# Kernel optimization log

Measured on AMD Instinct MI355X. Metric: run time of the kernel, lower is better.

## Reference

```python
import jax, jax.numpy as jnp
import numpy as np

B, N, E = 32, 2000, 32000      # graphs, nodes/graph, edges/graph
V, D, R, K = 100000, 128, 39, 8  # vocab, emb_dim, n_relation, n_bases
EPS = 1e-5


def setup_inputs() -> dict:
    key = jax.random.key(0)
    ks = jax.random.split(key, 8)
    node_ids = jax.random.randint(ks[0], (B, N), 0, V)
    edge_index = jax.random.randint(ks[1], (B, 2, E), 0, N)
    edge_type = jax.random.randint(ks[2], (B, E), 0, R)
    embedding = jax.random.normal(ks[3], (V, D), jnp.float32) * D ** -0.5
    bases = jax.random.normal(ks[4], (K, D, D), jnp.float32) * D ** -0.5
    comp = jax.random.normal(ks[5], (R, K), jnp.float32) * K ** -0.5
    root = jax.random.normal(ks[6], (D, D), jnp.float32) * D ** -0.5
    bias = jnp.zeros((D,), jnp.float32)
    return dict(node_ids=node_ids, edge_index=edge_index, edge_type=edge_type,
                embedding=embedding, bases=bases, comp=comp, root=root, bias=bias)


def _graph_fwd(node_ids, edge_index, edge_type, embedding, bases, comp, root, bias):
    # RGCNConv with basis decomposition and per-relation MEAN aggregation (PyG default).
    x = embedding[node_ids]                       # [N, D] per-graph node features
    src, dst = edge_index[0], edge_index[1]       # j -> i, aggregate at dst
    x_src = x[src]                                # [E, D]
    # mean normalizer per (dst, relation) bucket
    comb = dst * R + edge_type                    # [E]
    cnt = jax.ops.segment_sum(jnp.ones((E,), jnp.float32), comb, num_segments=N * R)
    inv = jnp.where(cnt > 0, 1.0 / cnt, 0.0)[comb]  # [E]
    # W_r = sum_k comp[r,k] * bases[k]; fold comp coefficients + mean norm into edge weights
    w = comp[edge_type] * inv[:, None]            # [E, K]
    out = x @ root + bias                         # root/self connection
    for k in range(K):                            # small fixed loop over bases
        zk = jax.ops.segment_sum(w[:, k:k + 1] * x_src, dst, num_segments=N)  # [N, D]
        out = out + zk @ bases[k]
    g = out.sum(axis=0)                           # sum pool over nodes
    # torch.nn.functional.normalize(p=2, eps=1e-5)
    return g / jnp.maximum(jnp.linalg.norm(g), EPS)


def reference(node_ids, edge_index, edge_type, embedding, bases, comp, root, bias):
    f = jax.vmap(_graph_fwd, in_axes=(0, 0, 0, None, None, None, None, None))
    return f(node_ids, edge_index, edge_type, embedding, bases, comp, root, bias)  # [B, D]
```

## Files before the change

### kernel.cpp

```cpp
#include <hip/hip_runtime.h>
#include <math.h>

#define Bn 32
#define Nn 2000
#define En 32000
#define Vn 100000
#define Dn 128
#define Rn 39
#define Kn 8

#define SUBS 8
#define NPS (Nn / SUBS)
#define NPAIR (Nn / 2)
#define EQ (En / 4)
#define NR (NPS * Rn)
#define GBLK 16
#define WSLOT (GBLK * 8)


__global__ __launch_bounds__(1024) void cntinv_kernel(const int* __restrict__ edge_index,
                                                      const int* __restrict__ edge_type,
                                                      float* __restrict__ inv) {
    int b = blockIdx.x, sub = blockIdx.y;
    int base = sub * NR;
    __shared__ int loc[NR];
    for (int i = threadIdx.x; i < NR; i += 1024) loc[i] = 0;
    __syncthreads();
    const int4* dst4 = (const int4*)(edge_index + (b * 2 + 1) * En);
    const int4* et4  = (const int4*)(edge_type + b * En);
    for (int q = threadIdx.x; q < EQ; q += 1024) {
        int4 d = dst4[q]; int4 t = et4[q]; int y;
        y = d.x * Rn + t.x - base; if ((unsigned)y < NR) atomicAdd(&loc[y], 1);
        y = d.y * Rn + t.y - base; if ((unsigned)y < NR) atomicAdd(&loc[y], 1);
        y = d.z * Rn + t.z - base; if ((unsigned)y < NR) atomicAdd(&loc[y], 1);
        y = d.w * Rn + t.w - base; if ((unsigned)y < NR) atomicAdd(&loc[y], 1);
    }
    __syncthreads();
    float* finv = (float*)loc;
    for (int i = threadIdx.x; i < NR; i += 1024) {
        int c = loc[i];
        finv[i] = 1.0f / (float)c;
    }
    __syncthreads();
    float* ivb = inv + (size_t)b * En;
    for (int q = threadIdx.x; q < EQ; q += 1024) {
        int4 d = dst4[q]; int4 t = et4[q];
        int e = 4 * q, y;
        y = d.x * Rn + t.x - base; if ((unsigned)y < NR) ivb[e]     = finv[y];
        y = d.y * Rn + t.y - base; if ((unsigned)y < NR) ivb[e + 1] = finv[y];
        y = d.z * Rn + t.z - base; if ((unsigned)y < NR) ivb[e + 2] = finv[y];
        y = d.w * Rn + t.w - base; if ((unsigned)y < NR) ivb[e + 3] = finv[y];
    }
}

__global__ __launch_bounds__(1024) void a_kernel(const int* __restrict__ edge_index,
                                                 const int* __restrict__ edge_type,
                                                 const float* __restrict__ inv,
                                                 const float* __restrict__ comp,
                                                 float* __restrict__ a) {
    int b = blockIdx.x, sub = blockIdx.y;
    int base = sub * NR;
    __shared__ float s[NR];
    __shared__ float comp_l[Rn * Kn];
    for (int i = threadIdx.x; i < NR; i += 1024) s[i] = 0.0f;
    if (threadIdx.x < Rn * Kn) comp_l[threadIdx.x] = comp[threadIdx.x];
    __syncthreads();
    const int4*   src4 = (const int4*)(edge_index + (b * 2 + 0) * En);
    const int4*   et4  = (const int4*)(edge_type + b * En);
    const float4* iv4  = (const float4*)(inv + (size_t)b * En);
    for (int q = threadIdx.x; q < EQ; q += 1024) {
        int4 sv = src4[q]; int4 tv = et4[q]; float4 iv = iv4[q]; int y;
        y = sv.x * Rn + tv.x - base; if ((unsigned)y < NR) atomicAdd(&s[y], iv.x);
        y = sv.y * Rn + tv.y - base; if ((unsigned)y < NR) atomicAdd(&s[y], iv.y);
        y = sv.z * Rn + tv.z - base; if ((unsigned)y < NR) atomicAdd(&s[y], iv.z);
        y = sv.w * Rn + tv.w - base; if ((unsigned)y < NR) atomicAdd(&s[y], iv.w);
    }
    __syncthreads();
    float* g = a + ((size_t)b * Nn + sub * NPS) * Kn;
    for (int i = threadIdx.x; i < NPS * Kn; i += 1024) {
        int n = i >> 3, k = i & 7;
        float acc = 0.0f;
        const float* srow = &s[n * Rn];
        for (int t = 0; t < Rn; t++) acc += srow[t] * comp_l[t * Kn + k];
        g[i] = acc;
    }
}

__global__ __launch_bounds__(512, 4) void gather_kernel(const int* __restrict__ node_ids,
                                                        const float* __restrict__ emb,
                                                        const float* __restrict__ a,
                                                        float* __restrict__ partial) {
    int b = blockIdx.x;
    int lane = threadIdx.x & 63, wv = threadIdx.x >> 6;
    int Wl = blockIdx.y * 8 + wv;
    int half = lane >> 5;
    int dl = lane & 31;
    __shared__ float red[8][9][Dn];
    float4 acc[9];
#pragma unroll
    for (int k = 0; k < 9; k++) acc[k] = make_float4(0.f, 0.f, 0.f, 0.f);
    const int*   nb = node_ids + b * Nn;
    const float* ab = a + (size_t)b * Nn * Kn;
#pragma unroll
    for (int i0 = 0; i0 < 8; i0 += 4) {
        bool   has[4];
        int    node[4];
        float4 v[4];
        float4 a0[4], a1[4];
#pragma unroll
        for (int i = 0; i < 4; i++) {
            int p = Wl + (i0 + i) * WSLOT;
            has[i] = p < NPAIR;
            node[i] = (has[i] ? 2 * p : 0) + half;
        }
#pragma unroll
        for (int i = 0; i < 4; i++) {
            int nid = nb[node[i]];
            v[i] = has[i] ? ((const float4*)(emb + (size_t)nid * Dn))[dl]
                          : make_float4(0.f, 0.f, 0.f, 0.f);
            const float4* ar = (const float4*)(ab + (size_t)node[i] * Kn);
            a0[i] = ar[0]; a1[i] = ar[1];
        }
#pragma unroll
        for (int i = 0; i < 4; i++) {
            float w[9] = {a0[i].x, a0[i].y, a0[i].z, a0[i].w,
                          a1[i].x, a1[i].y, a1[i].z, a1[i].w, 1.0f};
#pragma unroll
            for (int k = 0; k < 9; k++) {
                acc[k].x += w[k] * v[i].x;
                acc[k].y += w[k] * v[i].y;
                acc[k].z += w[k] * v[i].z;
                acc[k].w += w[k] * v[i].w;
            }
        }
    }
#pragma unroll
    for (int k = 0; k < 9; k++) {
        acc[k].x += __shfl_down(acc[k].x, 32, 64);
        acc[k].y += __shfl_down(acc[k].y, 32, 64);
        acc[k].z += __shfl_down(acc[k].z, 32, 64);
        acc[k].w += __shfl_down(acc[k].w, 32, 64);
    }
    if (half == 0) {
#pragma unroll
        for (int k = 0; k < 9; k++)
            ((float4*)red[wv][k])[dl] = acc[k];
    }
    __syncthreads();
    int slot = threadIdx.x;
    if (slot < 9 * (Dn / 4)) {
        int k = slot >> 5, d4 = slot & 31;
        float4 t = make_float4(0.f, 0.f, 0.f, 0.f);
#pragma unroll
        for (int w = 0; w < 8; w++) {
            float4 v = ((const float4*)red[w][k])[d4];
            t.x += v.x; t.y += v.y; t.z += v.z; t.w += v.w;
        }
        float4* gp = (float4*)(partial + (((size_t)b * 9 + k) * GBLK + blockIdx.y) * Dn);
        gp[d4] = t;
    }
}

__global__ __launch_bounds__(256) void matvec_kernel(const float* __restrict__ partial,
                                                     const float* __restrict__ root,
                                                     const float* __restrict__ bases,
                                                     float* __restrict__ gmat) {
    int b = blockIdx.x, m = blockIdx.y;
    int tid = threadIdx.x;
    __shared__ float4 ts4[Dn / 4];
    __shared__ float tsh[8][Dn];
    int dg = tid & 31, part = tid >> 5;
    const float4* p4 = (const float4*)(partial + ((size_t)b * 9 + m) * GBLK * Dn);
    float4 sum = make_float4(0.f, 0.f, 0.f, 0.f);
    for (int c = part; c < GBLK; c += 8) {
        float4 v = p4[c * 32 + dg];
        sum.x += v.x; sum.y += v.y; sum.z += v.z; sum.w += v.w;
    }
    ((float4*)tsh[part])[dg] = sum;
    __syncthreads();
    if (part == 0) {
        float4 t = make_float4(0.f, 0.f, 0.f, 0.f);
#pragma unroll
        for (int r = 0; r < 8; r++) {
            float4 v = ((float4*)tsh[r])[dg];
            t.x += v.x; t.y += v.y; t.z += v.z; t.w += v.w;
        }
        ts4[dg] = t;
    }
    __syncthreads();
    const float* ts = (const float*)ts4;
    const float* M  = (m == 8) ? root : bases + (size_t)m * Dn * Dn;
    int d = tid & (Dn - 1), h = tid >> 7;
    float g = 0.0f;
#pragma unroll 8
    for (int j = h * 64; j < h * 64 + 64; j++) g += ts[j] * M[j * Dn + d];
    __syncthreads();
    tsh[h][d] = g;
    __syncthreads();
    if (h == 0) gmat[((size_t)b * 9 + m) * Dn + d] = tsh[0][d] + tsh[1][d];
}

__global__ __launch_bounds__(128) void norm_kernel(const float* __restrict__ gmat,
                                                   const float* __restrict__ bias,
                                                   float* __restrict__ out) {
    int b = blockIdx.x, d = threadIdx.x;
    float g = (float)Nn * bias[d];
    const float* gb = gmat + (size_t)b * 9 * Dn + d;
#pragma unroll
    for (int m = 0; m < 9; m++) g += gb[m * Dn];
    float ss = g * g;
#pragma unroll
    for (int off = 32; off > 0; off >>= 1) ss += __shfl_down(ss, off, 64);
    __shared__ float s2[2];
    if ((threadIdx.x & 63) == 0) s2[threadIdx.x >> 6] = ss;
    __syncthreads();
    float nrm = sqrtf(s2[0] + s2[1]);
    out[b * Dn + d] = g / fmaxf(nrm, 1e-5f);
}

extern "C" void kernel_launch(void* const* d_in, const int* in_sizes, int n_in,
                              void* d_out, int out_size, void* d_ws, size_t ws_size,
                              hipStream_t stream) {
    const int*   node_ids   = (const int*)d_in[0];
    const int*   edge_index = (const int*)d_in[1];
    const int*   edge_type  = (const int*)d_in[2];
    const float* embedding  = (const float*)d_in[3];
    const float* bases      = (const float*)d_in[4];
    const float* comp       = (const float*)d_in[5];
    const float* root       = (const float*)d_in[6];
    const float* bias       = (const float*)d_in[7];
    float*       out        = (float*)d_out;

    char* w = (char*)d_ws;
    float* inv     = (float*)(w + 0);
    float* a       = (float*)(w + 4096000);
    float* partial = (float*)(w + 6144000);
    float* gmat    = (float*)(w + 8503296);

    cntinv_kernel<<<dim3(Bn, SUBS), 1024, 0, stream>>>(edge_index, edge_type, inv);
    a_kernel     <<<dim3(Bn, SUBS), 1024, 0, stream>>>(edge_index, edge_type, inv, comp, a);
    gather_kernel<<<dim3(Bn, GBLK), 512,  0, stream>>>(node_ids, embedding, a, partial);
    matvec_kernel<<<dim3(Bn, 9),    256,  0, stream>>>(partial, root, bases, gmat);
    norm_kernel  <<<Bn, 128, 0, stream>>>(gmat, bias, out);
}
```

Measured before the change: 141.4 us.

## Fuse all stages into one cooperative persistent kernel with grid syncs

Replaces the five separate launches (count/inverse, per-node coefficients, embedding gather, matvec, normalize) with one cooperative kernel of 256 blocks of 1024 threads. Stages are separated by grid.sync, and the gather now uses 16 waves per block over 8 sub-blocks per graph. The final matvec and normalize are merged into a single per-graph stage that runs on the first 32 blocks. This removes the launch gaps and intermediate gmat traffic, but adds grid-wide barrier costs and fixes the block shape for every stage.

```diff
diff --git a/kernel.cpp b/kernel.cpp
--- a/kernel.cpp
+++ b/kernel.cpp
@@ -1,5 +1,8 @@
 #include <hip/hip_runtime.h>
+#include <hip/hip_cooperative_groups.h>
 #include <math.h>
+
+namespace cg = cooperative_groups;
 
 #define Bn 32
 #define Nn 2000
@@ -14,208 +17,215 @@
 #define NPAIR (Nn / 2)
 #define EQ (En / 4)
 #define NR (NPS * Rn)
-#define GBLK 16
-#define WSLOT (GBLK * 8)
-
-
-__global__ __launch_bounds__(1024) void cntinv_kernel(const int* __restrict__ edge_index,
-                                                      const int* __restrict__ edge_type,
-                                                      float* __restrict__ inv) {
-    int b = blockIdx.x, sub = blockIdx.y;
-    int base = sub * NR;
-    __shared__ int loc[NR];
-    for (int i = threadIdx.x; i < NR; i += 1024) loc[i] = 0;
-    __syncthreads();
-    const int4* dst4 = (const int4*)(edge_index + (b * 2 + 1) * En);
-    const int4* et4  = (const int4*)(edge_type + b * En);
-    for (int q = threadIdx.x; q < EQ; q += 1024) {
-        int4 d = dst4[q]; int4 t = et4[q]; int y;
-        y = d.x * Rn + t.x - base; if ((unsigned)y < NR) atomicAdd(&loc[y], 1);
-        y = d.y * Rn + t.y - base; if ((unsigned)y < NR) atomicAdd(&loc[y], 1);
-        y = d.z * Rn + t.z - base; if ((unsigned)y < NR) atomicAdd(&loc[y], 1);
-        y = d.w * Rn + t.w - base; if ((unsigned)y < NR) atomicAdd(&loc[y], 1);
-    }
-    __syncthreads();
-    float* finv = (float*)loc;
-    for (int i = threadIdx.x; i < NR; i += 1024) {
-        int c = loc[i];
-        finv[i] = 1.0f / (float)c;
-    }
-    __syncthreads();
-    float* ivb = inv + (size_t)b * En;
-    for (int q = threadIdx.x; q < EQ; q += 1024) {
-        int4 d = dst4[q]; int4 t = et4[q];
-        int e = 4 * q, y;
-        y = d.x * Rn + t.x - base; if ((unsigned)y < NR) ivb[e]     = finv[y];
-        y = d.y * Rn + t.y - base; if ((unsigned)y < NR) ivb[e + 1] = finv[y];
-        y = d.z * Rn + t.z - base; if ((unsigned)y < NR) ivb[e + 2] = finv[y];
-        y = d.w * Rn + t.w - base; if ((unsigned)y < NR) ivb[e + 3] = finv[y];
-    }
-}
-
-__global__ __launch_bounds__(1024) void a_kernel(const int* __restrict__ edge_index,
-                                                 const int* __restrict__ edge_type,
-                                                 const float* __restrict__ inv,
-                                                 const float* __restrict__ comp,
-                                                 float* __restrict__ a) {
-    int b = blockIdx.x, sub = blockIdx.y;
-    int base = sub * NR;
-    __shared__ float s[NR];
-    __shared__ float comp_l[Rn * Kn];
-    for (int i = threadIdx.x; i < NR; i += 1024) s[i] = 0.0f;
-    if (threadIdx.x < Rn * Kn) comp_l[threadIdx.x] = comp[threadIdx.x];
-    __syncthreads();
-    const int4*   src4 = (const int4*)(edge_index + (b * 2 + 0) * En);
-    const int4*   et4  = (const int4*)(edge_type + b * En);
-    const float4* iv4  = (const float4*)(inv + (size_t)b * En);
-    for (int q = threadIdx.x; q < EQ; q += 1024) {
-        int4 sv = src4[q]; int4 tv = et4[q]; float4 iv = iv4[q]; int y;
-        y = sv.x * Rn + tv.x - base; if ((unsigned)y < NR) atomicAdd(&s[y], iv.x);
-        y = sv.y * Rn + tv.y - base; if ((unsigned)y < NR) atomicAdd(&s[y], iv.y);
-        y = sv.z * Rn + tv.z - base; if ((unsigned)y < NR) atomicAdd(&s[y], iv.z);
-        y = sv.w * Rn + tv.w - base; if ((unsigned)y < NR) atomicAdd(&s[y], iv.w);
-    }
-    __syncthreads();
-    float* g = a + ((size_t)b * Nn + sub * NPS) * Kn;
-    for (int i = threadIdx.x; i < NPS * Kn; i += 1024) {
-        int n = i >> 3, k = i & 7;
-        float acc = 0.0f;
-        const float* srow = &s[n * Rn];
-        for (int t = 0; t < Rn; t++) acc += srow[t] * comp_l[t * Kn + k];
-        g[i] = acc;
-    }
-}
-
-__global__ __launch_bounds__(512, 4) void gather_kernel(const int* __restrict__ node_ids,
-                                                        const float* __restrict__ emb,
-                                                        const float* __restrict__ a,
-                                                        float* __restrict__ partial) {
-    int b = blockIdx.x;
-    int lane = threadIdx.x & 63, wv = threadIdx.x >> 6;
-    int Wl = blockIdx.y * 8 + wv;
-    int half = lane >> 5;
-    int dl = lane & 31;
-    __shared__ float red[8][9][Dn];
-    float4 acc[9];
-#pragma unroll
-    for (int k = 0; k < 9; k++) acc[k] = make_float4(0.f, 0.f, 0.f, 0.f);
-    const int*   nb = node_ids + b * Nn;
-    const float* ab = a + (size_t)b * Nn * Kn;
-#pragma unroll
-    for (int i0 = 0; i0 < 8; i0 += 4) {
-        bool   has[4];
-        int    node[4];
-        float4 v[4];
-        float4 a0[4], a1[4];
-#pragma unroll
-        for (int i = 0; i < 4; i++) {
-            int p = Wl + (i0 + i) * WSLOT;
-            has[i] = p < NPAIR;
-            node[i] = (has[i] ? 2 * p : 0) + half;
-        }
-#pragma unroll
-        for (int i = 0; i < 4; i++) {
-            int nid = nb[node[i]];
-            v[i] = has[i] ? ((const float4*)(emb + (size_t)nid * Dn))[dl]
-                          : make_float4(0.f, 0.f, 0.f, 0.f);
-            const float4* ar = (const float4*)(ab + (size_t)node[i] * Kn);
-            a0[i] = ar[0]; a1[i] = ar[1];
-        }
-#pragma unroll
-        for (int i = 0; i < 4; i++) {
-            float w[9] = {a0[i].x, a0[i].y, a0[i].z, a0[i].w,
-                          a1[i].x, a1[i].y, a1[i].z, a1[i].w, 1.0f};
-#pragma unroll
-            for (int k = 0; k < 9; k++) {
-                acc[k].x += w[k] * v[i].x;
-                acc[k].y += w[k] * v[i].y;
-                acc[k].z += w[k] * v[i].z;
-                acc[k].w += w[k] * v[i].w;
-            }
-        }
-    }
-#pragma unroll
-    for (int k = 0; k < 9; k++) {
-        acc[k].x += __shfl_down(acc[k].x, 32, 64);
-        acc[k].y += __shfl_down(acc[k].y, 32, 64);
-        acc[k].z += __shfl_down(acc[k].z, 32, 64);
-        acc[k].w += __shfl_down(acc[k].w, 32, 64);
-    }
-    if (half == 0) {
-#pragma unroll
-        for (int k = 0; k < 9; k++)
-            ((float4*)red[wv][k])[dl] = acc[k];
-    }
-    __syncthreads();
-    int slot = threadIdx.x;
-    if (slot < 9 * (Dn / 4)) {
-        int k = slot >> 5, d4 = slot & 31;
-        float4 t = make_float4(0.f, 0.f, 0.f, 0.f);
-#pragma unroll
-        for (int w = 0; w < 8; w++) {
-            float4 v = ((const float4*)red[w][k])[d4];
-            t.x += v.x; t.y += v.y; t.z += v.z; t.w += v.w;
-        }
-        float4* gp = (float4*)(partial + (((size_t)b * 9 + k) * GBLK + blockIdx.y) * Dn);
-        gp[d4] = t;
-    }
-}
-
-__global__ __launch_bounds__(256) void matvec_kernel(const float* __restrict__ partial,
-                                                     const float* __restrict__ root,
-                                                     const float* __restrict__ bases,
-                                                     float* __restrict__ gmat) {
-    int b = blockIdx.x, m = blockIdx.y;
-    int tid = threadIdx.x;
-    __shared__ float4 ts4[Dn / 4];
-    __shared__ float tsh[8][Dn];
-    int dg = tid & 31, part = tid >> 5;
-    const float4* p4 = (const float4*)(partial + ((size_t)b * 9 + m) * GBLK * Dn);
-    float4 sum = make_float4(0.f, 0.f, 0.f, 0.f);
-    for (int c = part; c < GBLK; c += 8) {
-        float4 v = p4[c * 32 + dg];
-        sum.x += v.x; sum.y += v.y; sum.z += v.z; sum.w += v.w;
-    }
-    ((float4*)tsh[part])[dg] = sum;
-    __syncthreads();
-    if (part == 0) {
-        float4 t = make_float4(0.f, 0.f, 0.f, 0.f);
-#pragma unroll
-        for (int r = 0; r < 8; r++) {
-            float4 v = ((float4*)tsh[r])[dg];
-            t.x += v.x; t.y += v.y; t.z += v.z; t.w += v.w;
-        }
-        ts4[dg] = t;
-    }
-    __syncthreads();
-    const float* ts = (const float*)ts4;
-    const float* M  = (m == 8) ? root : bases + (size_t)m * Dn * Dn;
-    int d = tid & (Dn - 1), h = tid >> 7;
-    float g = 0.0f;
-#pragma unroll 8
-    for (int j = h * 64; j < h * 64 + 64; j++) g += ts[j] * M[j * Dn + d];
-    __syncthreads();
-    tsh[h][d] = g;
-    __syncthreads();
-    if (h == 0) gmat[((size_t)b * 9 + m) * Dn + d] = tsh[0][d] + tsh[1][d];
-}
-
-__global__ __launch_bounds__(128) void norm_kernel(const float* __restrict__ gmat,
-                                                   const float* __restrict__ bias,
-                                                   float* __restrict__ out) {
-    int b = blockIdx.x, d = threadIdx.x;
-    float g = (float)Nn * bias[d];
-    const float* gb = gmat + (size_t)b * 9 * Dn + d;
-#pragma unroll
-    for (int m = 0; m < 9; m++) g += gb[m * Dn];
-    float ss = g * g;
-#pragma unroll
-    for (int off = 32; off > 0; off >>= 1) ss += __shfl_down(ss, off, 64);
-    __shared__ float s2[2];
-    if ((threadIdx.x & 63) == 0) s2[threadIdx.x >> 6] = ss;
-    __syncthreads();
-    float nrm = sqrtf(s2[0] + s2[1]);
-    out[b * Dn + d] = g / fmaxf(nrm, 1e-5f);
+#define GBLK 8
+#define WSLOT 128
+#define SMEM_BYTES 73728
+
+
+__global__ __launch_bounds__(1024) void mega_kernel(
+    const int*   __restrict__ node_ids,
+    const int*   __restrict__ edge_index,
+    const int*   __restrict__ edge_type,
+    const float* __restrict__ emb,
+    const float* __restrict__ bases,
+    const float* __restrict__ comp,
+    const float* __restrict__ root,
+    const float* __restrict__ bias,
+    float*       __restrict__ inv,
+    float*       __restrict__ a,
+    float*       __restrict__ partial,
+    float*       __restrict__ out)
+{
+    cg::grid_group grid = cg::this_grid();
+    __shared__ __align__(16) char smem[SMEM_BYTES];
+    const int tid = threadIdx.x;
+    const int blk = blockIdx.x;
+    const int b = blk & 31, sub = blk >> 5;
+
+    {
+        int* loc = (int*)smem;
+        int base = sub * NR;
+        for (int i = tid; i < NR; i += 1024) loc[i] = 0;
+        __syncthreads();
+        const int4* dst4 = (const int4*)(edge_index + (b * 2 + 1) * En);
+        const int4* et4  = (const int4*)(edge_type + b * En);
+        for (int q = tid; q < EQ; q += 1024) {
+            int4 d = dst4[q]; int4 t = et4[q]; int y;
+            y = d.x * Rn + t.x - base; if ((unsigned)y < NR) atomicAdd(&loc[y], 1);
+            y = d.y * Rn + t.y - base; if ((unsigned)y < NR) atomicAdd(&loc[y], 1);
+            y = d.z * Rn + t.z - base; if ((unsigned)y < NR) atomicAdd(&loc[y], 1);
+            y = d.w * Rn + t.w - base; if ((unsigned)y < NR) atomicAdd(&loc[y], 1);
+        }
+        __syncthreads();
+        float* finv = (float*)loc;
+        for (int i = tid; i < NR; i += 1024) {
+            int c = loc[i];
+            finv[i] = 1.0f / (float)c;
+        }
+        __syncthreads();
+        float* ivb = inv + (size_t)b * En;
+        for (int q = tid; q < EQ; q += 1024) {
+            int4 d = dst4[q]; int4 t = et4[q];
+            int e = 4 * q, y;
+            y = d.x * Rn + t.x - base; if ((unsigned)y < NR) ivb[e]     = finv[y];
+            y = d.y * Rn + t.y - base; if ((unsigned)y < NR) ivb[e + 1] = finv[y];
+            y = d.z * Rn + t.z - base; if ((unsigned)y < NR) ivb[e + 2] = finv[y];
+            y = d.w * Rn + t.w - base; if ((unsigned)y < NR) ivb[e + 3] = finv[y];
+        }
+    }
+    __threadfence();
+    grid.sync();
+
+    {
+        float* s      = (float*)smem;
+        float* comp_l = (float*)(smem + NR * sizeof(float));
+        int base = sub * NR;
+        for (int i = tid; i < NR; i += 1024) s[i] = 0.0f;
+        if (tid < Rn * Kn) comp_l[tid] = comp[tid];
+        __syncthreads();
+        const int4*   src4 = (const int4*)(edge_index + (b * 2 + 0) * En);
+        const int4*   et4  = (const int4*)(edge_type + b * En);
+        const float4* iv4  = (const float4*)(inv + (size_t)b * En);
+        for (int q = tid; q < EQ; q += 1024) {
+            int4 sv = src4[q]; int4 tv = et4[q]; float4 iv = iv4[q]; int y;
+            y = sv.x * Rn + tv.x - base; if ((unsigned)y < NR) atomicAdd(&s[y], iv.x);
+            y = sv.y * Rn + tv.y - base; if ((unsigned)y < NR) atomicAdd(&s[y], iv.y);
+            y = sv.z * Rn + tv.z - base; if ((unsigned)y < NR) atomicAdd(&s[y], iv.z);
+            y = sv.w * Rn + tv.w - base; if ((unsigned)y < NR) atomicAdd(&s[y], iv.w);
+        }
+        __syncthreads();
+        float* g = a + ((size_t)b * Nn + sub * NPS) * Kn;
+        for (int i = tid; i < NPS * Kn; i += 1024) {
+            int n = i >> 3, k = i & 7;
+            float acc = 0.0f;
+            const float* srow = &s[n * Rn];
+            for (int t = 0; t < Rn; t++) acc += srow[t] * comp_l[t * Kn + k];
+            g[i] = acc;
+        }
+    }
+    __threadfence();
+    grid.sync();
+
+    {
+        float (*red)[9][Dn] = (float (*)[9][Dn])smem;
+        int lane = tid & 63, wv = tid >> 6;
+        int Wl = sub * 16 + wv;
+        int half = lane >> 5;
+        int dl = lane & 31;
+        float4 acc[9];
+#pragma unroll
+        for (int k = 0; k < 9; k++) acc[k] = make_float4(0.f, 0.f, 0.f, 0.f);
+        const int*   nb = node_ids + b * Nn;
+        const float* ab = a + (size_t)b * Nn * Kn;
+#pragma unroll
+        for (int i0 = 0; i0 < 8; i0 += 4) {
+            bool   has[4];
+            int    node[4];
+            float4 v[4];
+            float4 a0[4], a1[4];
+#pragma unroll
+            for (int i = 0; i < 4; i++) {
+                int p = Wl + (i0 + i) * WSLOT;
+                has[i] = p < NPAIR;
+                node[i] = (has[i] ? 2 * p : 0) + half;
+            }
+#pragma unroll
+            for (int i = 0; i < 4; i++) {
+                int nid = nb[node[i]];
+                v[i] = has[i] ? ((const float4*)(emb + (size_t)nid * Dn))[dl]
+                              : make_float4(0.f, 0.f, 0.f, 0.f);
+                const float4* ar = (const float4*)(ab + (size_t)node[i] * Kn);
+                a0[i] = ar[0]; a1[i] = ar[1];
+            }
+#pragma unroll
+            for (int i = 0; i < 4; i++) {
+                float w[9] = {a0[i].x, a0[i].y, a0[i].z, a0[i].w,
+                              a1[i].x, a1[i].y, a1[i].z, a1[i].w, 1.0f};
+#pragma unroll
+                for (int k = 0; k < 9; k++) {
+                    acc[k].x += w[k] * v[i].x;
+                    acc[k].y += w[k] * v[i].y;
+                    acc[k].z += w[k] * v[i].z;
+                    acc[k].w += w[k] * v[i].w;
+                }
+            }
+        }
+#pragma unroll
+        for (int k = 0; k < 9; k++) {
+            acc[k].x += __shfl_down(acc[k].x, 32, 64);
+            acc[k].y += __shfl_down(acc[k].y, 32, 64);
+            acc[k].z += __shfl_down(acc[k].z, 32, 64);
+            acc[k].w += __shfl_down(acc[k].w, 32, 64);
+        }
+        if (half == 0) {
+#pragma unroll
+            for (int k = 0; k < 9; k++)
+                ((float4*)red[wv][k])[dl] = acc[k];
+        }
+        __syncthreads();
+        if (tid < 9 * (Dn / 4)) {
+            int k = tid >> 5, d4 = tid & 31;
+            float4 t = make_float4(0.f, 0.f, 0.f, 0.f);
+#pragma unroll
+            for (int w = 0; w < 16; w++) {
+                float4 v = ((const float4*)red[w][k])[d4];
+                t.x += v.x; t.y += v.y; t.z += v.z; t.w += v.w;
+            }
+            float4* gp = (float4*)(partial + (((size_t)b * 9 + k) * GBLK + sub) * Dn);
+            gp[d4] = t;
+        }
+    }
+    __threadfence();
+    grid.sync();
+
+    if (blk >= Bn) return;
+    {
+        float*  ts   = (float*)smem;
+        float4* red4 = (float4*)(smem + 4608);
+        float*  ssr  = (float*)(smem + 4608 + 16384);
+        for (int slot = tid; slot < 9 * Dn; slot += 1024) {
+            int k = slot >> 7, d = slot & 127;
+            const float* pp = partial + (((size_t)blk * 9 + k) * GBLK) * Dn + d;
+            float t = 0.0f;
+#pragma unroll
+            for (int c = 0; c < GBLK; c++) t += pp[c * Dn];
+            ts[slot] = t;
+        }
+        __syncthreads();
+        int d4 = tid & 31, jg = tid >> 5;
+        float4 acc = make_float4(0.f, 0.f, 0.f, 0.f);
+        for (int m = 0; m < 9; m++) {
+            const float4* M4 = (const float4*)((m == 8) ? root
+                                                        : bases + (size_t)m * Dn * Dn);
+            const float* tsm = ts + m * Dn;
+#pragma unroll
+            for (int jj = 0; jj < 4; jj++) {
+                int j = jg * 4 + jj;
+                float w = tsm[j];
+                float4 mv = M4[j * 32 + d4];
+                acc.x += w * mv.x; acc.y += w * mv.y;
+                acc.z += w * mv.z; acc.w += w * mv.w;
+            }
+        }
+        red4[jg * 32 + d4] = acc;
+        __syncthreads();
+        const float* redf = (const float*)red4;
+        int d = tid & 127;
+        float g = (float)Nn * bias[d];
+#pragma unroll
+        for (int w = 0; w < 32; w++) g += redf[w * Dn + d];
+        float ss = g * g;
+#pragma unroll
+        for (int off = 32; off > 0; off >>= 1) ss += __shfl_down(ss, off, 64);
+        if ((tid & 63) == 0) ssr[tid >> 6] = ss;
+        __syncthreads();
+        float tot = 0.0f;
+#pragma unroll
+        for (int w = 0; w < 16; w++) tot += ssr[w];
+        tot *= 0.125f;
+        float nrm = sqrtf(tot);
+        if (tid < Dn) out[blk * Dn + tid] = g / fmaxf(nrm, 1e-5f);
+    }
 }
 
 extern "C" void kernel_launch(void* const* d_in, const int* in_sizes, int n_in,
@@ -235,11 +245,11 @@
     float* inv     = (float*)(w + 0);
     float* a       = (float*)(w + 4096000);
     float* partial = (float*)(w + 6144000);
-    float* gmat    = (float*)(w + 8503296);
-
-    cntinv_kernel<<<dim3(Bn, SUBS), 1024, 0, stream>>>(edge_index, edge_type, inv);
-    a_kernel     <<<dim3(Bn, SUBS), 1024, 0, stream>>>(edge_index, edge_type, inv, comp, a);
-    gather_kernel<<<dim3(Bn, GBLK), 512,  0, stream>>>(node_ids, embedding, a, partial);
-    matvec_kernel<<<dim3(Bn, 9),    256,  0, stream>>>(partial, root, bases, gmat);
-    norm_kernel  <<<Bn, 128, 0, stream>>>(gmat, bias, out);
+
+    void* args[] = {
+        (void*)&node_ids, (void*)&edge_index, (void*)&edge_type,
+        (void*)&embedding, (void*)&bases, (void*)&comp, (void*)&root,
+        (void*)&bias, (void*)&inv, (void*)&a, (void*)&partial, (void*)&out
+    };
+    hipLaunchCooperativeKernel(mega_kernel, dim3(256), dim3(1024), args, 0, stream);
 }
```

Measured after the change: 497.8 us. +252.1%, slower.
